# Kernel tuning notes

Measured on AMD Instinct MI355X. Metric: run time of the kernel, lower is better.

Reference implementation:

```python
import jax, jax.numpy as jnp
import numpy as np

N, NFEAT, NHID, NCLASS, NHEAD = 8192, 512, 64, 16, 4
ALPHA = 0.1  # leaky relu slope
NEG = -9e15


def setup_inputs() -> dict:
    key = jax.random.key(0)
    ks = jax.random.split(key, 7)
    x = jax.random.normal(ks[0], (N, NFEAT), dtype=jnp.float32)
    adj = (jax.random.uniform(ks[1], (N, N)) < 0.05).astype(jnp.float32)
    # per-head params: W [H, nfeat, nhid], a [H, 2*nhid] (xavier-ish scale)
    W = jax.random.normal(ks[2], (NHEAD, NFEAT, NHID), dtype=jnp.float32) * (1.0 / np.sqrt(NFEAT))
    a = jax.random.normal(ks[3], (NHEAD, 2 * NHID), dtype=jnp.float32) * (1.0 / np.sqrt(NHID))
    W_out = jax.random.normal(ks[4], (NHEAD * NHID, NCLASS), dtype=jnp.float32) * (1.0 / np.sqrt(NHEAD * NHID))
    a_out = jax.random.normal(ks[5], (2 * NCLASS,), dtype=jnp.float32) * (1.0 / np.sqrt(NCLASS))
    return {"x": x, "adj": adj, "W": W, "a": a, "W_out": W_out, "a_out": a_out}


def _gat_layer(h, adj, Wk, ak):
    """Dense pyGAT GraphAttentionLayer (eval mode, dropout = identity)."""
    d = Wk.shape[1]
    Wh = h @ Wk                         # [N, d]
    f1 = Wh @ ak[:d]                    # [N]
    f2 = Wh @ ak[d:]                    # [N]
    e = jax.nn.leaky_relu(f1[:, None] + f2[None, :], negative_slope=ALPHA)  # [N, N]
    att = jax.nn.softmax(jnp.where(adj > 0, e, NEG), axis=1)
    return att @ Wh                     # [N, d]


def reference(x, adj, W, a, W_out, a_out):
    # eval mode: F.dropout is identity
    heads = jax.vmap(lambda Wk, ak: jax.nn.elu(_gat_layer(x, adj, Wk, ak)))(W, a)  # [H, N, nhid]
    h = jnp.transpose(heads, (1, 0, 2)).reshape(x.shape[0], -1)                    # [N, H*nhid]
    out = jax.nn.elu(_gat_layer(h, adj, W_out, a_out))                             # [N, nclass]
    return jax.nn.log_softmax(out, axis=1)
```

## Files before the change

kernel.cpp:

```cpp
#include <hip/hip_runtime.h>
#include <hip/hip_bf16.h>

#define NN 8192
#define NFEAT 512
#define NHID 64
#define NCLASS 16
#define NHEAD 4
#define ALPHA 0.1f
#define ZSPLIT 4
#define JPB (NN / ZSPLIT)
#define DCH 128
#define Z2 8
#define JPB2 (NN / Z2)

typedef short bf16x8 __attribute__((ext_vector_type(8)));
typedef float f32x4 __attribute__((ext_vector_type(4)));
typedef float fv4 __attribute__((ext_vector_type(4)));

__device__ __forceinline__ float lrelu(float x) { return fmaxf(x, ALPHA * x); }
__device__ __forceinline__ float elu(float x) { return x > 0.f ? x : __expf(x) - 1.f; }
__device__ __forceinline__ short f2b(float x) {
  union { __bf16 b; short s; } c; c.b = (__bf16)x; return c.s;
}
__device__ __forceinline__ float b2f(short x) {
  union { unsigned int u; float f; } c; c.u = ((unsigned int)(unsigned short)x) << 16; return c.f;
}
__device__ __forceinline__ unsigned int fkey(float f) {
  const unsigned int b = __float_as_uint(f);
  return (b & 0x80000000u) ? ~b : (b | 0x80000000u);
}
__device__ __forceinline__ float funkey(unsigned int k) {
  const unsigned int b = (k & 0x80000000u) ? (k & 0x7fffffffu) : ~k;
  return __uint_as_float(b);
}

__global__ __launch_bounds__(256) void k_wprep(const float* __restrict__ W,
                                               short* __restrict__ WB) {
  __shared__ float t[64][65];
  const int h = blockIdx.y;
  const int k0 = blockIdx.x * 64;
  const int tid = threadIdx.x;
#pragma unroll
  for (int it = 0; it < 16; ++it) {
    const int r = it * 4 + (tid >> 6), c = tid & 63;
    t[r][c] = W[((size_t)h * NFEAT + k0 + r) * NHID + c];
  }
  __syncthreads();
#pragma unroll
  for (int it = 0; it < 16; ++it) {
    const int d = it * 4 + (tid >> 6), k = tid & 63;
    WB[((size_t)h * NHID + d) * NFEAT + k0 + k] = f2b(t[k][d]);
  }
}

__global__ __launch_bounds__(256) void k_prep1(const float* __restrict__ x,
                                               const short* __restrict__ WB,
                                               const float* __restrict__ a,
                                               short* __restrict__ Whf,
                                               float* __restrict__ f1i,
                                               float* __restrict__ f2i,
                                               unsigned int* __restrict__ f2maxK) {
  __shared__ short tile[64][72];
  __shared__ float bmx[4];
  const int bid = blockIdx.x;
  const int h = bid >> 7;
  const int bm = (bid & 127) * 64;
  const int tid = threadIdx.x;
  const int wv = tid >> 6, lane = tid & 63;
  const int mr = lane & 15, kg = lane >> 4;
  f32x4 acc0 = {0.f, 0.f, 0.f, 0.f}, acc1 = acc0, acc2 = acc0, acc3 = acc0;
  const float* ap = x + (size_t)(bm + wv * 16 + mr) * NFEAT + kg * 8;
  const short* bp = WB + ((size_t)h * NHID + mr) * NFEAT + kg * 8;
#pragma unroll 2
  for (int k0 = 0; k0 < NFEAT; k0 += 32) {
    const float4 xa = *reinterpret_cast<const float4*>(ap);
    const float4 xb = *reinterpret_cast<const float4*>(ap + 4);
    bf16x8 af;
    af[0] = f2b(xa.x); af[1] = f2b(xa.y); af[2] = f2b(xa.z); af[3] = f2b(xa.w);
    af[4] = f2b(xb.x); af[5] = f2b(xb.y); af[6] = f2b(xb.z); af[7] = f2b(xb.w);
    const bf16x8 b0 = *reinterpret_cast<const bf16x8*>(bp);
    const bf16x8 b1 = *reinterpret_cast<const bf16x8*>(bp + 16 * NFEAT);
    const bf16x8 b2 = *reinterpret_cast<const bf16x8*>(bp + 32 * NFEAT);
    const bf16x8 b3 = *reinterpret_cast<const bf16x8*>(bp + 48 * NFEAT);
    acc0 = __builtin_amdgcn_mfma_f32_16x16x32_bf16(af, b0, acc0, 0, 0, 0);
    acc1 = __builtin_amdgcn_mfma_f32_16x16x32_bf16(af, b1, acc1, 0, 0, 0);
    acc2 = __builtin_amdgcn_mfma_f32_16x16x32_bf16(af, b2, acc2, 0, 0, 0);
    acc3 = __builtin_amdgcn_mfma_f32_16x16x32_bf16(af, b3, acc3, 0, 0, 0);
    ap += 32; bp += 32;
  }
  float a1v[4], a2v[4];
#pragma unroll
  for (int c = 0; c < 4; ++c) {
    a1v[c] = a[h * 128 + mr + c * 16];
    a2v[c] = a[h * 128 + 64 + mr + c * 16];
  }
  float m2 = -1e30f;
#pragma unroll
  for (int q = 0; q < 4; ++q) {
    float s1 = acc0[q] * a1v[0] + acc1[q] * a1v[1] + acc2[q] * a1v[2] + acc3[q] * a1v[3];
    float s2 = acc0[q] * a2v[0] + acc1[q] * a2v[1] + acc2[q] * a2v[2] + acc3[q] * a2v[3];
#pragma unroll
    for (int off = 1; off < 16; off <<= 1) {
      s1 += __shfl_xor(s1, off);
      s2 += __shfl_xor(s2, off);
    }
    m2 = fmaxf(m2, s2);
    if (mr == 0) {
      const int i = bm + wv * 16 + kg * 4 + q;
      f1i[(size_t)i * 4 + h] = s1;
      f2i[(size_t)i * 4 + h] = s2;
    }
  }
  m2 = fmaxf(m2, __shfl_xor(m2, 16));
  m2 = fmaxf(m2, __shfl_xor(m2, 32));
  if (lane == 0) bmx[wv] = m2;
#pragma unroll
  for (int q = 0; q < 4; ++q) {
    const int r = wv * 16 + kg * 4 + q;
    tile[r][mr +  0] = f2b(acc0[q]);
    tile[r][mr + 16] = f2b(acc1[q]);
    tile[r][mr + 32] = f2b(acc2[q]);
    tile[r][mr + 48] = f2b(acc3[q]);
  }
  __syncthreads();
  if (tid == 0)
    atomicMax(f2maxK + h, fkey(fmaxf(fmaxf(bmx[0], bmx[1]), fmaxf(bmx[2], bmx[3]))));
#pragma unroll
  for (int it = 0; it < 2; ++it) {
    const int jbl = (tid >> 6) + it * 4;
    const int d = tid & 63;
    bf16x8 o;
#pragma unroll
    for (int jo = 0; jo < 8; ++jo) o[jo] = tile[jbl * 8 + jo][d];
    *reinterpret_cast<bf16x8*>(Whf +
        (((size_t)h * 1024 + (bm >> 3) + jbl) * 64 + d) * 8) = o;
  }
}

__global__ __launch_bounds__(256) void k_acbd(const float* __restrict__ f1i,
                                              const float* __restrict__ f2i,
                                              const unsigned int* __restrict__ f2maxK,
                                              float2* __restrict__ ACh,
                                              unsigned int* __restrict__ BDh) {
  const int idx = blockIdx.x * 256 + threadIdx.x;
  const int i = idx & (NN - 1);
  const int h = idx >> 13;
  const float fm = funkey(f2maxK[h]);
  const float f1 = f1i[(size_t)i * 4 + h];
  const float f2 = f2i[(size_t)i * 4 + h];
  const float s = f1 + fm;
  const float mrow = fmaxf(s, 0.1f * s);
  float2 ac;
  ac.x = __expf(s - mrow);
  ac.y = __expf(0.1f * s - mrow);
  ACh[(size_t)h * NN + i] = ac;
  const float t = f2 - fm;
  const unsigned int B = (unsigned short)f2b(__expf(t));
  const unsigned int D = (unsigned short)f2b(__expf(0.1f * t));
  BDh[(size_t)h * NN + i] = B | (D << 16);
}

__global__ __launch_bounds__(256) void k_acbd2(const float* __restrict__ f1o,
                                               const float* __restrict__ f2o,
                                               const unsigned int* __restrict__ f2omaxK,
                                               float2* __restrict__ AC2,
                                               unsigned int* __restrict__ BD2) {
  const int i = blockIdx.x * 256 + threadIdx.x;
  const float fm = funkey(f2omaxK[0]);
  const float f1 = f1o[i];
  const float f2 = f2o[i];
  const float s = f1 + fm;
  const float mrow = fmaxf(s, 0.1f * s);
  float2 ac;
  ac.x = __expf(s - mrow);
  ac.y = __expf(0.1f * s - mrow);
  AC2[i] = ac;
  const float t = f2 - fm;
  const unsigned int B = (unsigned short)f2b(__expf(t));
  const unsigned int D = (unsigned short)f2b(__expf(0.1f * t));
  BD2[i] = B | (D << 16);
}

__global__ __launch_bounds__(256) void k_scan(const float* __restrict__ adj,
                                              unsigned int* __restrict__ bmask) {
  const fv4* a4 = reinterpret_cast<const fv4*>(adj);
  const int t0 = blockIdx.x * 256 + threadIdx.x;
#pragma unroll 4
  for (int it = 0; it < 32; ++it) {
    const int g = it * 524288 + t0;
    const fv4 v = __builtin_nontemporal_load(a4 + g);
    unsigned int nv = (unsigned int)((v.x > 0.f) | ((v.y > 0.f) << 1) |
                                     ((v.z > 0.f) << 2) | ((v.w > 0.f) << 3))
                      << ((threadIdx.x & 7) * 4);
    nv |= __shfl_xor(nv, 1);
    nv |= __shfl_xor(nv, 2);
    nv |= __shfl_xor(nv, 4);
    if ((threadIdx.x & 7) == 0) bmask[g >> 3] = nv;
  }
}

__global__ __launch_bounds__(256) void k_dense1z(const unsigned int* __restrict__ bmask,
                                                 const short* __restrict__ Whf,
                                                 const float2* __restrict__ ACh,
                                                 const unsigned int* __restrict__ BDh,
                                                 float* __restrict__ OpP,
                                                 float* __restrict__ rsP) {
  __shared__ short sm_b[16 * 64 * 8];
  __shared__ unsigned int sm_bd[DCH];
  __shared__ unsigned int sm_mask[64][5];
  const int i0 = blockIdx.x * 64;
  const int h = blockIdx.y;
  const int z = blockIdx.z;
  const int jb0 = z * JPB;
  const int tid = threadIdx.x;
  const int wv = tid >> 6, lane = tid & 63;
  const int mr = lane & 15, kg = lane >> 4;
  const int row_local = wv * 16 + mr;
  const float2 ac = ACh[(size_t)h * NN + i0 + row_local];
  f32x4 acc0 = {0.f, 0.f, 0.f, 0.f}, acc1 = acc0, acc2 = acc0, acc3 = acc0;
  float rs = 0.f;
  const int NCH = JPB / DCH;

  unsigned int rM, rBD;
  uint4 rB0, rB1, rB2, rB3;
#define LOADR(jc)                                                              \
  {                                                                            \
    rM = bmask[(size_t)(i0 + (tid >> 2)) * 256 + ((jc) >> 5) + (tid & 3)];     \
    rBD = BDh[(size_t)h * NN + (jc) + (tid & (DCH - 1))];                      \
    const uint4* src_ = reinterpret_cast<const uint4*>(                       \
        Whf + ((size_t)h * 1024 + ((jc) >> 3)) * 512);                         \
    rB0 = src_[tid];                                                           \
    rB1 = src_[tid + 256];                                                     \
    rB2 = src_[tid + 512];                                                     \
    rB3 = src_[tid + 768];                                                     \
  }
  LOADR(jb0)
  for (int c = 0; c < NCH; ++c) {
    __syncthreads();
    sm_mask[tid >> 2][tid & 3] = rM;
    if (tid < DCH) sm_bd[tid] = rBD;
    {
      uint4* dst = reinterpret_cast<uint4*>(sm_b);
      dst[tid] = rB0; dst[tid + 256] = rB1; dst[tid + 512] = rB2; dst[tid + 768] = rB3;
    }
    if (c + 1 < NCH) LOADR(jb0 + (c + 1) * DCH)
    __syncthreads();
#pragma unroll
    for (int ks = 0; ks < DCH / 32; ++ks) {
      const int jl = ks * 32 + kg * 8;
      const uint4 bda = *reinterpret_cast<const uint4*>(&sm_bd[jl]);
      const uint4 bdb = *reinterpret_cast<const uint4*>(&sm_bd[jl + 4]);
      const unsigned int mbb = (sm_mask[row_local][ks] >> (kg * 8)) & 0xffu;
      bf16x8 af;
#define MKW(e, bdw)                                              \
      {                                                          \
        const float Bf = __uint_as_float((bdw) << 16);           \
        const float Df = __uint_as_float((bdw) & 0xffff0000u);   \
        float w_ = fmaxf(ac.x * Bf, ac.y * Df);                  \
        w_ = ((mbb >> (e)) & 1u) ? w_ : 0.f;                     \
        rs += w_;                                                \
        af[e] = f2b(w_);                                         \
      }
      MKW(0, bda.x) MKW(1, bda.y) MKW(2, bda.z) MKW(3, bda.w)
      MKW(4, bdb.x) MKW(5, bdb.y) MKW(6, bdb.z) MKW(7, bdb.w)
#undef MKW
      const short* wp = sm_b + ((size_t)(jl >> 3) * 64 + mr) * 8;
      const bf16x8 bf0 = *reinterpret_cast<const bf16x8*>(wp);
      const bf16x8 bf1 = *reinterpret_cast<const bf16x8*>(wp + 128);
      const bf16x8 bf2 = *reinterpret_cast<const bf16x8*>(wp + 256);
      const bf16x8 bf3 = *reinterpret_cast<const bf16x8*>(wp + 384);
      acc0 = __builtin_amdgcn_mfma_f32_16x16x32_bf16(af, bf0, acc0, 0, 0, 0);
      acc1 = __builtin_amdgcn_mfma_f32_16x16x32_bf16(af, bf1, acc1, 0, 0, 0);
      acc2 = __builtin_amdgcn_mfma_f32_16x16x32_bf16(af, bf2, acc2, 0, 0, 0);
      acc3 = __builtin_amdgcn_mfma_f32_16x16x32_bf16(af, bf3, acc3, 0, 0, 0);
    }
  }
#undef LOADR
  rs += __shfl_xor(rs, 16);
  rs += __shfl_xor(rs, 32);
  if (lane < 16)
    rsP[((size_t)z * NHEAD + h) * NN + i0 + wv * 16 + lane] = rs;
  float* op = OpP + (((size_t)z * NHEAD + h) * NN + i0) * 64;
#pragma unroll
  for (int q = 0; q < 4; ++q) {
    const int r = wv * 16 + kg * 4 + q;
    op[(size_t)r * 64 + mr +  0] = acc0[q];
    op[(size_t)r * 64 + mr + 16] = acc1[q];
    op[(size_t)r * 64 + mr + 32] = acc2[q];
    op[(size_t)r * 64 + mr + 48] = acc3[q];
  }
}

__global__ __launch_bounds__(256) void k_comb1(const float* __restrict__ OpP,
                                               const float* __restrict__ rsP,
                                               short* __restrict__ hcat) {
  const int idx = blockIdx.x * 256 + threadIdx.x;
  const int i = idx >> 8;
  const int hc = idx & 255;
  const int h = hc >> 6, d = hc & 63;
  float s = 0.f, rsum = 0.f;
#pragma unroll
  for (int z = 0; z < ZSPLIT; ++z) {
    s += OpP[(((size_t)z * NHEAD + h) * NN + i) * 64 + d];
    rsum += rsP[((size_t)z * NHEAD + h) * NN + i];
  }
  hcat[idx] = f2b(elu(s / rsum));
}

__global__ __launch_bounds__(256) void k_gemm2(const short* __restrict__ hcat,
                                               const float* __restrict__ Wout,
                                               const float* __restrict__ aout,
                                               short* __restrict__ Wh2f,
                                               float* __restrict__ f1o,
                                               float* __restrict__ f2o,
                                               unsigned int* __restrict__ f2omaxK) {
  __shared__ float sW[NHEAD * NHID][NCLASS + 1];
  __shared__ float sh[16][NHEAD * NHID + 1];
  __shared__ float bmx[4];
  const int tid = threadIdx.x;
  const int r = tid >> 4, c = tid & 15;
  const int row = blockIdx.x * 16 + r;
  for (int u = tid; u < 256 * 16; u += 256) sW[u >> 4][u & 15] = Wout[u];
  for (int u = tid; u < 16 * 256; u += 256)
    sh[u >> 8][u & 255] = b2f(hcat[(size_t)(blockIdx.x * 16 + (u >> 8)) * 256 + (u & 255)]);
  __syncthreads();
  float acc = 0.f;
#pragma unroll 8
  for (int f = 0; f < 256; ++f) acc += sh[r][f] * sW[f][c];
  Wh2f[(((size_t)blockIdx.x * 2 + (r >> 3)) * 16 + c) * 8 + (r & 7)] = f2b(acc);
  float s1 = acc * aout[c];
  float s2 = acc * aout[NCLASS + c];
#pragma unroll
  for (int off = 8; off; off >>= 1) { s1 += __shfl_xor(s1, off); s2 += __shfl_xor(s2, off); }
  if (c == 0) { f1o[row] = s1; f2o[row] = s2; }
  float m2 = s2;
  m2 = fmaxf(m2, __shfl_xor(m2, 16));
  m2 = fmaxf(m2, __shfl_xor(m2, 32));
  if ((tid & 63) == 0) bmx[tid >> 6] = m2;
  __syncthreads();
  if (tid == 0)
    atomicMax(f2omaxK, fkey(fmaxf(fmaxf(bmx[0], bmx[1]), fmaxf(bmx[2], bmx[3]))));
}

__global__ __launch_bounds__(256) void k_dense2z(const unsigned int* __restrict__ bmask,
                                                 const short* __restrict__ Wh2f,
                                                 const float2* __restrict__ AC2,
                                                 const unsigned int* __restrict__ BD2,
                                                 float* __restrict__ Op2P,
                                                 float* __restrict__ rs2P) {
  __shared__ unsigned int sm_mask[64][33];
  const int i0 = blockIdx.x * 64;
  const int z = blockIdx.y;
  const int jb0 = z * JPB2;
  const int tid = threadIdx.x;
  {
    const int row = tid >> 2;
    const int w0 = (tid & 3) * 8;
#pragma unroll
    for (int u = 0; u < 8; ++u)
      sm_mask[row][w0 + u] = bmask[(size_t)(i0 + row) * 256 + (jb0 >> 5) + w0 + u];
  }
  __syncthreads();
  const int wv = tid >> 6, lane = tid & 63;
  const int mr = lane & 15, kg = lane >> 4;
  const int row_local = wv * 16 + mr;
  const float2 ac = AC2[i0 + row_local];
  f32x4 acc = {0.f, 0.f, 0.f, 0.f};
  float rs = 0.f;
  const unsigned int* bd = BD2 + jb0;
  const short* w2 = Wh2f + (size_t)(jb0 >> 3) * 128 + mr * 8;
#pragma unroll 2
  for (int ks = 0; ks < 32; ++ks) {
    const int jl = ks * 32 + kg * 8;
    const uint4 bda = *reinterpret_cast<const uint4*>(bd + jl);
    const uint4 bdb = *reinterpret_cast<const uint4*>(bd + jl + 4);
    const unsigned int mbb = (sm_mask[row_local][ks] >> (kg * 8)) & 0xffu;
    bf16x8 af;
#define MKW(e, bdw)                                              \
    {                                                            \
      const float Bf = __uint_as_float((bdw) << 16);             \
      const float Df = __uint_as_float((bdw) & 0xffff0000u);     \
      float w_ = fmaxf(ac.x * Bf, ac.y * Df);                    \
      w_ = ((mbb >> (e)) & 1u) ? w_ : 0.f;                       \
      rs += w_;                                                  \
      af[e] = f2b(w_);                                           \
    }
    MKW(0, bda.x) MKW(1, bda.y) MKW(2, bda.z) MKW(3, bda.w)
    MKW(4, bdb.x) MKW(5, bdb.y) MKW(6, bdb.z) MKW(7, bdb.w)
#undef MKW
    const bf16x8 bf = *reinterpret_cast<const bf16x8*>(w2 + (size_t)(jl >> 3) * 128);
    acc = __builtin_amdgcn_mfma_f32_16x16x32_bf16(af, bf, acc, 0, 0, 0);
  }
  rs += __shfl_xor(rs, 16);
  rs += __shfl_xor(rs, 32);
  if (lane < 16)
    rs2P[(size_t)z * NN + i0 + wv * 16 + lane] = rs;
  float* op = Op2P + ((size_t)z * NN + i0) * NCLASS;
#pragma unroll
  for (int q = 0; q < 4; ++q)
    op[(size_t)(wv * 16 + kg * 4 + q) * NCLASS + mr] = acc[q];
}

__global__ __launch_bounds__(256) void k_comb2(const float* __restrict__ Op2P,
                                               const float* __restrict__ rs2P,
                                               float* __restrict__ out) {
  const int idx = blockIdx.x * 256 + threadIdx.x;
  const int i = idx >> 4;
  const int c = idx & 15;
  float s = 0.f, rsum = 0.f;
#pragma unroll
  for (int z = 0; z < Z2; ++z) {
    s += Op2P[((size_t)z * NN + i) * NCLASS + c];
    rsum += rs2P[(size_t)z * NN + i];
  }
  const float v = elu(s / rsum);
  float vm = v;
#pragma unroll
  for (int off = 8; off; off >>= 1) vm = fmaxf(vm, __shfl_xor(vm, off, 16));
  float ex = __expf(v - vm);
#pragma unroll
  for (int off = 8; off; off >>= 1) ex += __shfl_xor(ex, off, 16);
  out[idx] = v - vm - __logf(ex);
}

extern "C" void kernel_launch(void* const* d_in, const int* in_sizes, int n_in,
                              void* d_out, int out_size, void* d_ws, size_t ws_size,
                              hipStream_t stream) {
  const float* x    = (const float*)d_in[0];
  const float* adj  = (const float*)d_in[1];
  const float* W    = (const float*)d_in[2];
  const float* a    = (const float*)d_in[3];
  const float* Wout = (const float*)d_in[4];
  const float* aout = (const float*)d_in[5];
  float* out = (float*)d_out;
  char* ws = (char*)d_ws;
  const size_t MB = 1048576;
  const size_t KB = 1024;

  unsigned int* bmask  = (unsigned int*)(ws);
  short* Whf           = (short*)(ws + 8 * MB);
  short* hcat          = (short*)(ws + 12 * MB);
  float* OpP           = (float*)(ws + 16 * MB);
  float* rsP           = (float*)(ws + 48 * MB);
  float* Op2P          = (float*)(ws + 49 * MB);
  float* rs2P          = (float*)(ws + 53 * MB);
  short* WB            = (short*)(ws + 54 * MB);
  float* f1i           = (float*)(ws + 54 * MB + 256 * KB);
  float* f2i           = (float*)(ws + 54 * MB + 384 * KB);
  float2* ACh          = (float2*)(ws + 54 * MB + 512 * KB);
  unsigned int* BDh    = (unsigned int*)(ws + 54 * MB + 768 * KB);
  float* f1o           = (float*)(ws + 54 * MB + 896 * KB);
  float* f2o           = (float*)(ws + 54 * MB + 928 * KB);
  short* Wh2f          = (short*)(ws + 54 * MB + 960 * KB);
  float2* AC2          = (float2*)(ws + 54 * MB + 1216 * KB);
  unsigned int* BD2    = (unsigned int*)(ws + 54 * MB + 1280 * KB);
  unsigned int* f2maxK = (unsigned int*)(ws + 54 * MB + 1312 * KB);
  unsigned int* f2omaxK = f2maxK + 4;

  hipMemsetAsync(f2maxK, 0, 8 * sizeof(unsigned int), stream);
  k_wprep<<<dim3(8, 4), 256, 0, stream>>>(W, WB);
  k_prep1<<<512, 256, 0, stream>>>(x, WB, a, Whf, f1i, f2i, f2maxK);
  k_acbd<<<NN * NHEAD / 256, 256, 0, stream>>>(f1i, f2i, f2maxK, ACh, BDh);
  k_scan<<<2048, 256, 0, stream>>>(adj, bmask);
  k_dense1z<<<dim3(NN / 64, NHEAD, ZSPLIT), 256, 0, stream>>>(bmask, Whf, ACh, BDh, OpP, rsP);
  k_comb1<<<NN, 256, 0, stream>>>(OpP, rsP, hcat);
  k_gemm2<<<NN / 16, 256, 0, stream>>>(hcat, Wout, aout, Wh2f, f1o, f2o, f2omaxK);
  k_acbd2<<<NN / 256, 256, 0, stream>>>(f1o, f2o, f2omaxK, AC2, BD2);
  k_dense2z<<<dim3(NN / 64, Z2), 256, 0, stream>>>(bmask, Wh2f, AC2, BD2, Op2P, rs2P);
  k_comb2<<<NN * NCLASS / 256, 256, 0, stream>>>(Op2P, rs2P, out);
}
```

Baseline: 212.6 us.

## Fuse adjacency bitmask scan into layer-1 attention kernel with per-wave heads

Removes the separate adjacency scan kernel and folds the float-to-bitmask conversion into the layer-1 dense attention kernel. Each block now handles 32 rows, and each of its four waves handles one head, so the adjacency tile is read once and shared across heads. The bitmask is double-buffered in shared memory and still written out for layer 2. Wh and BD values are now loaded directly from global memory (cached) instead of staged through LDS, which trades LDS traffic and barriers for more global and L2 loads.

```diff
diff --git a/kernel.cpp b/kernel.cpp
--- a/kernel.cpp
+++ b/kernel.cpp
@@ -10,6 +10,8 @@
 #define ZSPLIT 4
 #define JPB (NN / ZSPLIT)
 #define DCH 128
+#define NCH (JPB / DCH)
+#define ROWS1 32
 #define Z2 8
 #define JPB2 (NN / Z2)
 
@@ -181,114 +183,161 @@
   BD2[i] = B | (D << 16);
 }
 
-__global__ __launch_bounds__(256) void k_scan(const float* __restrict__ adj,
-                                              unsigned int* __restrict__ bmask) {
-  const fv4* a4 = reinterpret_cast<const fv4*>(adj);
-  const int t0 = blockIdx.x * 256 + threadIdx.x;
-#pragma unroll 4
-  for (int it = 0; it < 32; ++it) {
-    const int g = it * 524288 + t0;
-    const fv4 v = __builtin_nontemporal_load(a4 + g);
-    unsigned int nv = (unsigned int)((v.x > 0.f) | ((v.y > 0.f) << 1) |
-                                     ((v.z > 0.f) << 2) | ((v.w > 0.f) << 3))
-                      << ((threadIdx.x & 7) * 4);
-    nv |= __shfl_xor(nv, 1);
-    nv |= __shfl_xor(nv, 2);
-    nv |= __shfl_xor(nv, 4);
-    if ((threadIdx.x & 7) == 0) bmask[g >> 3] = nv;
-  }
-}
-
-__global__ __launch_bounds__(256) void k_dense1z(const unsigned int* __restrict__ bmask,
-                                                 const short* __restrict__ Whf,
-                                                 const float2* __restrict__ ACh,
-                                                 const unsigned int* __restrict__ BDh,
-                                                 float* __restrict__ OpP,
-                                                 float* __restrict__ rsP) {
-  __shared__ short sm_b[16 * 64 * 8];
-  __shared__ unsigned int sm_bd[DCH];
-  __shared__ unsigned int sm_mask[64][5];
-  const int i0 = blockIdx.x * 64;
-  const int h = blockIdx.y;
-  const int z = blockIdx.z;
+__global__ __launch_bounds__(256, 4) void k_dense1f(const float* __restrict__ adj,
+                                                    const short* __restrict__ Whf,
+                                                    const float2* __restrict__ ACh,
+                                                    const unsigned int* __restrict__ BDh,
+                                                    float* __restrict__ OpP,
+                                                    float* __restrict__ rsP,
+                                                    unsigned int* __restrict__ bmask) {
+  __shared__ unsigned int smM[2][ROWS1][5];
+  const int i0 = blockIdx.x * ROWS1;
+  const int z = blockIdx.y;
   const int jb0 = z * JPB;
   const int tid = threadIdx.x;
   const int wv = tid >> 6, lane = tid & 63;
   const int mr = lane & 15, kg = lane >> 4;
-  const int row_local = wv * 16 + mr;
-  const float2 ac = ACh[(size_t)h * NN + i0 + row_local];
-  f32x4 acc0 = {0.f, 0.f, 0.f, 0.f}, acc1 = acc0, acc2 = acc0, acc3 = acc0;
-  float rs = 0.f;
-  const int NCH = JPB / DCH;
-
-  unsigned int rM, rBD;
-  uint4 rB0, rB1, rB2, rB3;
-#define LOADR(jc)                                                              \
-  {                                                                            \
-    rM = bmask[(size_t)(i0 + (tid >> 2)) * 256 + ((jc) >> 5) + (tid & 3)];     \
-    rBD = BDh[(size_t)h * NN + (jc) + (tid & (DCH - 1))];                      \
-    const uint4* src_ = reinterpret_cast<const uint4*>(                       \
-        Whf + ((size_t)h * 1024 + ((jc) >> 3)) * 512);                         \
-    rB0 = src_[tid];                                                           \
-    rB1 = src_[tid + 256];                                                     \
-    rB2 = src_[tid + 512];                                                     \
-    rB3 = src_[tid + 768];                                                     \
-  }
-  LOADR(jb0)
+  const int h = wv;
+  const int arow = tid >> 3;
+  const int aseg = tid & 7;
+  const float2 ac0 = ACh[(size_t)h * NN + i0 + mr];
+  const float2 ac1 = ACh[(size_t)h * NN + i0 + 16 + mr];
+  f32x4 acc[2][4];
+#pragma unroll
+  for (int mt = 0; mt < 2; ++mt)
+#pragma unroll
+    for (int dq = 0; dq < 4; ++dq) acc[mt][dq] = (f32x4){0.f, 0.f, 0.f, 0.f};
+  float rs0 = 0.f, rs1 = 0.f;
+  const unsigned int* bdh = BDh + (size_t)h * NN + jb0;
+  const short* whb = Whf + ((size_t)h * 1024 + (jb0 >> 3)) * 512 + mr * 8;
+
+  fv4 r0, r1, r2, r3;
+#define LOADADJ(c)                                                        \
+  {                                                                       \
+    const fv4* p_ = reinterpret_cast<const fv4*>(                         \
+        adj + (size_t)(i0 + arow) * NN + jb0 + (c) * DCH + aseg * 16);    \
+    r0 = __builtin_nontemporal_load(p_);                                  \
+    r1 = __builtin_nontemporal_load(p_ + 1);                              \
+    r2 = __builtin_nontemporal_load(p_ + 2);                              \
+    r3 = __builtin_nontemporal_load(p_ + 3);                              \
+  }
+#define CVTW(c, buf)                                                              \
+  {                                                                               \
+    unsigned int b_ =                                                             \
+        (unsigned int)(r0.x > 0.f)         | ((unsigned int)(r0.y > 0.f) << 1) |  \
+        ((unsigned int)(r0.z > 0.f) << 2)  | ((unsigned int)(r0.w > 0.f) << 3) |  \
+        ((unsigned int)(r1.x > 0.f) << 4)  | ((unsigned int)(r1.y > 0.f) << 5) |  \
+        ((unsigned int)(r1.z > 0.f) << 6)  | ((unsigned int)(r1.w > 0.f) << 7) |  \
+        ((unsigned int)(r2.x > 0.f) << 8)  | ((unsigned int)(r2.y > 0.f) << 9) |  \
+        ((unsigned int)(r2.z > 0.f) << 10) | ((unsigned int)(r2.w > 0.f) << 11) | \
+        ((unsigned int)(r3.x > 0.f) << 12) | ((unsigned int)(r3.y > 0.f) << 13) | \
+        ((unsigned int)(r3.z > 0.f) << 14) | ((unsigned int)(r3.w > 0.f) << 15);  \
+    unsigned int nv_ = b_ << ((aseg & 1) * 16);                                   \
+    nv_ |= __shfl_xor(nv_, 1);                                                    \
+    if ((aseg & 1) == 0) {                                                        \
+      smM[buf][arow][aseg >> 1] = nv_;                                            \
+      bmask[(size_t)(i0 + arow) * 256 + (jb0 >> 5) + (c) * 4 + (aseg >> 1)] = nv_;\
+    }                                                                             \
+  }
+#define MK8(mbb, acv, rsv, AF)                                   \
+  {                                                              \
+    const float B0 = __uint_as_float(bda.x << 16);               \
+    const float D0 = __uint_as_float(bda.x & 0xffff0000u);       \
+    const float B1 = __uint_as_float(bda.y << 16);               \
+    const float D1 = __uint_as_float(bda.y & 0xffff0000u);       \
+    const float B2 = __uint_as_float(bda.z << 16);               \
+    const float D2 = __uint_as_float(bda.z & 0xffff0000u);       \
+    const float B3 = __uint_as_float(bda.w << 16);               \
+    const float D3 = __uint_as_float(bda.w & 0xffff0000u);       \
+    const float B4 = __uint_as_float(bdb.x << 16);               \
+    const float D4 = __uint_as_float(bdb.x & 0xffff0000u);       \
+    const float B5 = __uint_as_float(bdb.y << 16);               \
+    const float D5 = __uint_as_float(bdb.y & 0xffff0000u);       \
+    const float B6 = __uint_as_float(bdb.z << 16);               \
+    const float D6 = __uint_as_float(bdb.z & 0xffff0000u);       \
+    const float B7 = __uint_as_float(bdb.w << 16);               \
+    const float D7 = __uint_as_float(bdb.w & 0xffff0000u);       \
+    float w0 = fmaxf((acv).x * B0, (acv).y * D0);                \
+    float w1 = fmaxf((acv).x * B1, (acv).y * D1);                \
+    float w2 = fmaxf((acv).x * B2, (acv).y * D2);                \
+    float w3 = fmaxf((acv).x * B3, (acv).y * D3);                \
+    float w4 = fmaxf((acv).x * B4, (acv).y * D4);                \
+    float w5 = fmaxf((acv).x * B5, (acv).y * D5);                \
+    float w6 = fmaxf((acv).x * B6, (acv).y * D6);                \
+    float w7 = fmaxf((acv).x * B7, (acv).y * D7);                \
+    w0 = ((mbb) & 1u)   ? w0 : 0.f;                              \
+    w1 = ((mbb) & 2u)   ? w1 : 0.f;                              \
+    w2 = ((mbb) & 4u)   ? w2 : 0.f;                              \
+    w3 = ((mbb) & 8u)   ? w3 : 0.f;                              \
+    w4 = ((mbb) & 16u)  ? w4 : 0.f;                              \
+    w5 = ((mbb) & 32u)  ? w5 : 0.f;                              \
+    w6 = ((mbb) & 64u)  ? w6 : 0.f;                              \
+    w7 = ((mbb) & 128u) ? w7 : 0.f;                              \
+    (rsv) += ((w0 + w1) + (w2 + w3)) + ((w4 + w5) + (w6 + w7));  \
+    AF[0] = f2b(w0); AF[1] = f2b(w1); AF[2] = f2b(w2);           \
+    AF[3] = f2b(w3); AF[4] = f2b(w4); AF[5] = f2b(w5);           \
+    AF[6] = f2b(w6); AF[7] = f2b(w7);                            \
+  }
+
+  LOADADJ(0)
+  CVTW(0, 0)
+  __syncthreads();
   for (int c = 0; c < NCH; ++c) {
-    __syncthreads();
-    sm_mask[tid >> 2][tid & 3] = rM;
-    if (tid < DCH) sm_bd[tid] = rBD;
-    {
-      uint4* dst = reinterpret_cast<uint4*>(sm_b);
-      dst[tid] = rB0; dst[tid + 256] = rB1; dst[tid + 512] = rB2; dst[tid + 768] = rB3;
-    }
-    if (c + 1 < NCH) LOADR(jb0 + (c + 1) * DCH)
-    __syncthreads();
-#pragma unroll
-    for (int ks = 0; ks < DCH / 32; ++ks) {
-      const int jl = ks * 32 + kg * 8;
-      const uint4 bda = *reinterpret_cast<const uint4*>(&sm_bd[jl]);
-      const uint4 bdb = *reinterpret_cast<const uint4*>(&sm_bd[jl + 4]);
-      const unsigned int mbb = (sm_mask[row_local][ks] >> (kg * 8)) & 0xffu;
-      bf16x8 af;
-#define MKW(e, bdw)                                              \
-      {                                                          \
-        const float Bf = __uint_as_float((bdw) << 16);           \
-        const float Df = __uint_as_float((bdw) & 0xffff0000u);   \
-        float w_ = fmaxf(ac.x * Bf, ac.y * Df);                  \
-        w_ = ((mbb >> (e)) & 1u) ? w_ : 0.f;                     \
-        rs += w_;                                                \
-        af[e] = f2b(w_);                                         \
-      }
-      MKW(0, bda.x) MKW(1, bda.y) MKW(2, bda.z) MKW(3, bda.w)
-      MKW(4, bdb.x) MKW(5, bdb.y) MKW(6, bdb.z) MKW(7, bdb.w)
-#undef MKW
-      const short* wp = sm_b + ((size_t)(jl >> 3) * 64 + mr) * 8;
+    if (c + 1 < NCH) LOADADJ(c + 1)
+    const int bsel = c & 1;
+#pragma unroll
+    for (int ks = 0; ks < 4; ++ks) {
+      const int jl = c * DCH + ks * 32 + kg * 8;
+      const uint4 bda = *reinterpret_cast<const uint4*>(bdh + jl);
+      const uint4 bdb = *reinterpret_cast<const uint4*>(bdh + jl + 4);
+      const short* wp = whb + (size_t)(jl >> 3) * 512;
       const bf16x8 bf0 = *reinterpret_cast<const bf16x8*>(wp);
       const bf16x8 bf1 = *reinterpret_cast<const bf16x8*>(wp + 128);
       const bf16x8 bf2 = *reinterpret_cast<const bf16x8*>(wp + 256);
       const bf16x8 bf3 = *reinterpret_cast<const bf16x8*>(wp + 384);
-      acc0 = __builtin_amdgcn_mfma_f32_16x16x32_bf16(af, bf0, acc0, 0, 0, 0);
-      acc1 = __builtin_amdgcn_mfma_f32_16x16x32_bf16(af, bf1, acc1, 0, 0, 0);
-      acc2 = __builtin_amdgcn_mfma_f32_16x16x32_bf16(af, bf2, acc2, 0, 0, 0);
-      acc3 = __builtin_amdgcn_mfma_f32_16x16x32_bf16(af, bf3, acc3, 0, 0, 0);
+      {
+        const unsigned int mbb = (smM[bsel][mr][ks] >> (kg * 8)) & 0xffu;
+        bf16x8 af;
+        MK8(mbb, ac0, rs0, af)
+        acc[0][0] = __builtin_amdgcn_mfma_f32_16x16x32_bf16(af, bf0, acc[0][0], 0, 0, 0);
+        acc[0][1] = __builtin_amdgcn_mfma_f32_16x16x32_bf16(af, bf1, acc[0][1], 0, 0, 0);
+        acc[0][2] = __builtin_amdgcn_mfma_f32_16x16x32_bf16(af, bf2, acc[0][2], 0, 0, 0);
+        acc[0][3] = __builtin_amdgcn_mfma_f32_16x16x32_bf16(af, bf3, acc[0][3], 0, 0, 0);
+      }
+      {
+        const unsigned int mbb = (smM[bsel][16 + mr][ks] >> (kg * 8)) & 0xffu;
+        bf16x8 af;
+        MK8(mbb, ac1, rs1, af)
+        acc[1][0] = __builtin_amdgcn_mfma_f32_16x16x32_bf16(af, bf0, acc[1][0], 0, 0, 0);
+        acc[1][1] = __builtin_amdgcn_mfma_f32_16x16x32_bf16(af, bf1, acc[1][1], 0, 0, 0);
+        acc[1][2] = __builtin_amdgcn_mfma_f32_16x16x32_bf16(af, bf2, acc[1][2], 0, 0, 0);
+        acc[1][3] = __builtin_amdgcn_mfma_f32_16x16x32_bf16(af, bf3, acc[1][3], 0, 0, 0);
+      }
     }
-  }
-#undef LOADR
-  rs += __shfl_xor(rs, 16);
-  rs += __shfl_xor(rs, 32);
-  if (lane < 16)
-    rsP[((size_t)z * NHEAD + h) * NN + i0 + wv * 16 + lane] = rs;
+    if (c + 1 < NCH) CVTW(c + 1, bsel ^ 1)
+    __syncthreads();
+  }
+#undef MK8
+#undef CVTW
+#undef LOADADJ
+  rs0 += __shfl_xor(rs0, 16); rs0 += __shfl_xor(rs0, 32);
+  rs1 += __shfl_xor(rs1, 16); rs1 += __shfl_xor(rs1, 32);
+  float* rsp = rsP + ((size_t)z * NHEAD + h) * NN + i0;
+  if (lane < 16) {
+    rsp[lane] = rs0;
+    rsp[16 + lane] = rs1;
+  }
   float* op = OpP + (((size_t)z * NHEAD + h) * NN + i0) * 64;
 #pragma unroll
-  for (int q = 0; q < 4; ++q) {
-    const int r = wv * 16 + kg * 4 + q;
-    op[(size_t)r * 64 + mr +  0] = acc0[q];
-    op[(size_t)r * 64 + mr + 16] = acc1[q];
-    op[(size_t)r * 64 + mr + 32] = acc2[q];
-    op[(size_t)r * 64 + mr + 48] = acc3[q];
-  }
+  for (int mt = 0; mt < 2; ++mt)
+#pragma unroll
+    for (int q = 0; q < 4; ++q) {
+      const int r = mt * 16 + kg * 4 + q;
+      op[(size_t)r * 64 + mr +  0] = acc[mt][0][q];
+      op[(size_t)r * 64 + mr + 16] = acc[mt][1][q];
+      op[(size_t)r * 64 + mr + 32] = acc[mt][2][q];
+      op[(size_t)r * 64 + mr + 48] = acc[mt][3][q];
+    }
 }
 
 __global__ __launch_bounds__(256) void k_comb1(const float* __restrict__ OpP,
@@ -461,8 +510,7 @@
   k_wprep<<<dim3(8, 4), 256, 0, stream>>>(W, WB);
   k_prep1<<<512, 256, 0, stream>>>(x, WB, a, Whf, f1i, f2i, f2maxK);
   k_acbd<<<NN * NHEAD / 256, 256, 0, stream>>>(f1i, f2i, f2maxK, ACh, BDh);
-  k_scan<<<2048, 256, 0, stream>>>(adj, bmask);
-  k_dense1z<<<dim3(NN / 64, NHEAD, ZSPLIT), 256, 0, stream>>>(bmask, Whf, ACh, BDh, OpP, rsP);
+  k_dense1f<<<dim3(NN / ROWS1, ZSPLIT), 256, 0, stream>>>(adj, Whf, ACh, BDh, OpP, rsP, bmask);
   k_comb1<<<NN, 256, 0, stream>>>(OpP, rsP, hcat);
   k_gemm2<<<NN / 16, 256, 0, stream>>>(hcat, Wout, aout, Wh2f, f1o, f2o, f2omaxK);
   k_acbd2<<<NN / 256, 256, 0, stream>>>(f1o, f2o, f2omaxK, AC2, BD2);
```

After: 463.1 us (median of 2 runs). 118% more time.
